# Performance work log

Measured on AMD Instinct MI355X. Metric: run time of the kernel, lower is better.

## Reference

```python
import jax, jax.numpy as jnp
import numpy as np

FRAME, PROJ, MID, HID, T, B = 2048, 512, 128, 1024, 48, 512


def _uniform(key, shape, stdv):
    return jax.random.uniform(key, shape, jnp.float32, -stdv, stdv)


def setup_inputs() -> dict:
    key = jax.random.key(0)
    ks = jax.random.split(key, 16)
    sp = 1.0 / np.sqrt(FRAME)   # frame_embed init
    s1 = 1.0 / np.sqrt(HID)     # LSTMCell init (1/sqrt(hidden))
    sbd = 1.0 / np.sqrt(PROJ)   # BoundaryDetector init (1/sqrt(i_features))
    return {
        "video_feats": jax.random.normal(ks[0], (B, T, FRAME), jnp.float32),
        # frame_embed: Linear(frame_size, projected_size)
        "We": _uniform(ks[1], (PROJ, FRAME), sp),
        "be": _uniform(ks[2], (PROJ,), sp),
        # lstm1: LSTMCell(projected, hidden) with bias
        "W1_ih": _uniform(ks[3], (4 * HID, PROJ), s1),
        "W1_hh": _uniform(ks[4], (4 * HID, HID), s1),
        "b1_ih": _uniform(ks[5], (4 * HID,), s1),
        "b1_hh": _uniform(ks[6], (4 * HID,), s1),
        # lstm2: LSTMCell(hidden, hidden), bias=False
        "W2_ih": _uniform(ks[7], (4 * HID, HID), s1),
        "W2_hh": _uniform(ks[8], (4 * HID, HID), s1),
        # BoundaryDetector params
        "Wsi": _uniform(ks[9], (MID, PROJ), sbd),
        "Wsh": _uniform(ks[10], (MID, HID), sbd),
        "bbd": _uniform(ks[11], (MID,), sbd),
        "vs": _uniform(ks[12], (1, MID), sbd),
    }


def _lstm_cell(x, h, c, W_ih, W_hh, b):
    gates = x @ W_ih.T + h @ W_hh.T + b  # [B, 4H]
    i, f, g, o = jnp.split(gates, 4, axis=-1)  # PyTorch gate order i,f,g,o
    i, f, o = jax.nn.sigmoid(i), jax.nn.sigmoid(f), jax.nn.sigmoid(o)
    g = jnp.tanh(g)
    c_new = f * c + i * g
    h_new = o * jnp.tanh(c_new)
    return h_new, c_new


def _binary_gate(z):
    # eval mode: threshold 0.5; straight-through identity backward
    hard = (z > 0.5).astype(z.dtype)
    return z + jax.lax.stop_gradient(hard - z)


def reference(video_feats, We, be, W1_ih, W1_hh, b1_ih, b1_hh, W2_ih, W2_hh, Wsi, Wsh, bbd, vs):
    bsz = video_feats.shape[0]
    # frame embedding (dropout is identity in eval mode)
    v = video_feats @ We.T + be  # [B, T, PROJ]
    v_t = jnp.swapaxes(v, 0, 1)  # [T, B, PROJ]
    b1 = b1_ih + b1_hh
    zeros = jnp.zeros((bsz, HID), video_feats.dtype)

    def step(carry, vt):
        h1, c1, h2, c2 = carry
        z = jax.nn.sigmoid((vt @ Wsi.T + h1 @ Wsh.T + bbd) @ vs.T)  # [B, 1]
        s = _binary_gate(z)
        h1n, c1n = _lstm_cell(vt, h1, c1, W1_ih, W1_hh, b1)
        h2n, c2n = _lstm_cell(h1n * s, h2, c2, W2_ih, W2_hh, 0.0)
        h1n = h1n * (1.0 - s)
        c1n = c1n * (1.0 - s)
        return (h1n, c1n, h2n, c2n), None

    (h1, _, _, _), _ = jax.lax.scan(step, (zeros, zeros, zeros, zeros), v_t)
    return h1
```

## Files before the change

kernel.cpp:

```cpp
#include <hip/hip_runtime.h>

#define B_     512
#define T_     48
#define FRAME_ 2048
#define PROJ_  512
#define MID_   128
#define HID_   1024
#define G4_    4096

typedef unsigned short u16;
typedef __bf16 bf16x8 __attribute__((ext_vector_type(8)));
typedef float  f32x4  __attribute__((ext_vector_type(4)));

__device__ __forceinline__ float sigmoidf_(float x) {
    return 1.0f / (1.0f + expf(-x));
}
__device__ __forceinline__ u16 f2bf_rn(float f) {
    unsigned int u = __float_as_uint(f);
    u += 0x7fffu + ((u >> 16) & 1u);
    return (u16)(u >> 16);
}
__device__ __forceinline__ float bf2f(u16 s) {
    return __uint_as_float(((unsigned int)s) << 16);
}
__device__ __forceinline__ void gld16(const void* g, void* l) {
    __builtin_amdgcn_global_load_lds((const __attribute__((address_space(1))) void*)g,
                                     (__attribute__((address_space(3))) void*)l, 16, 0, 0);
}
__device__ __forceinline__ uint4 pack8(const u16* h) {
    return make_uint4((unsigned)h[0] | ((unsigned)h[1] << 16),
                      (unsigned)h[2] | ((unsigned)h[3] << 16),
                      (unsigned)h[4] | ((unsigned)h[5] << 16),
                      (unsigned)h[6] | ((unsigned)h[7] << 16));
}

__global__ void wvec_kernel(const float* __restrict__ Wsi, const float* __restrict__ Wsh,
                            const float* __restrict__ vs,
                            double* __restrict__ wsi_vd, float* __restrict__ wsh_v)
{
    const int gid = blockIdx.x * 256 + threadIdx.x;
    if (gid < 512) {
        double s = 0.0;
        for (int mi = 0; mi < MID_; ++mi)
            s += (double)vs[mi] * (double)Wsi[(size_t)mi * PROJ_ + gid];
        wsi_vd[gid] = s;
    } else if (gid < 1536) {
        const int k = gid - 512;
        double s = 0.0;
        for (int mi = 0; mi < MID_; ++mi)
            s += (double)vs[mi] * (double)Wsh[(size_t)mi * HID_ + k];
        wsh_v[k] = (float)s;
    }
}

__global__ void cc_kernel(const float* __restrict__ be, const double* __restrict__ wsi_vd,
                          const float* __restrict__ vs, const float* __restrict__ bbd,
                          double* __restrict__ cc)
{
    __shared__ double red[256];
    const int tid = threadIdx.x;
    double s = 0.0;
    for (int p = tid; p < PROJ_; p += 256) s += (double)be[p] * wsi_vd[p];
    red[tid] = s;
    __syncthreads();
    for (int st = 128; st > 0; st >>= 1) {
        if (tid < st) red[tid] += red[tid + st];
        __syncthreads();
    }
    if (tid == 0) {
        double b = 0.0;
        for (int mi = 0; mi < MID_; ++mi) b += (double)vs[mi] * (double)bbd[mi];
        cc[0] = red[0] + b;
    }
}

__global__ void u_kernel(const float* __restrict__ We, const double* __restrict__ wsi_vd,
                         double* __restrict__ u)
{
    const int f = blockIdx.x * 256 + threadIdx.x;
    double s = 0.0;
    for (int p = 0; p < PROJ_; ++p)
        s += wsi_vd[p] * (double)We[(size_t)p * FRAME_ + f];
    u[f] = s;
}

__global__ __launch_bounds__(256)
void vidpack_kernel(const float* __restrict__ video, const double* __restrict__ u,
                    const double* __restrict__ cc,
                    u16* __restrict__ phi, u16* __restrict__ plo,
                    float* __restrict__ Lv)
{
    __shared__ double red[16][17];
    const int tid = threadIdx.x;
    const int r   = tid & 15, kq = tid >> 4;
    const int row = blockIdx.x * 16 + r;
    const float* vr = video + (size_t)row * FRAME_;
    double s = 0.0;
#pragma unroll
    for (int j = 0; j < 16; ++j) {
        const int k0 = kq * 128 + j * 8;
        const float4 a = *(const float4*)&vr[k0];
        const float4 b = *(const float4*)&vr[k0 + 4];
        const float f[8] = {a.x, a.y, a.z, a.w, b.x, b.y, b.z, b.w};
        s += (double)f[0]*u[k0+0] + (double)f[1]*u[k0+1] + (double)f[2]*u[k0+2]
           + (double)f[3]*u[k0+3] + (double)f[4]*u[k0+4] + (double)f[5]*u[k0+5]
           + (double)f[6]*u[k0+6] + (double)f[7]*u[k0+7];
        u16 h[8], l[8];
#pragma unroll
        for (int e = 0; e < 8; ++e) {
            h[e] = f2bf_rn(f[e]);
            l[e] = f2bf_rn(f[e] - bf2f(h[e]));
        }
        const int g = kq * 16 + j;
        const size_t off = ((size_t)g * 24576 + row) * 16;
        *(uint4*)((char*)phi + off) = pack8(h);
        *(uint4*)((char*)plo + off) = pack8(l);
    }
    red[r][kq] = s;
    __syncthreads();
    if (tid < 16) {
        double t = 0.0;
#pragma unroll
        for (int q = 0; q < 16; ++q) t += red[tid][q];
        const int rw = blockIdx.x * 16 + tid;
        Lv[(rw % T_) * B_ + rw / T_] = (float)(t + cc[0]);
    }
}

__global__ void wepack_kernel(const float* __restrict__ We,
                              u16* __restrict__ phi, u16* __restrict__ plo)
{
    const int kk = blockIdx.x, by = blockIdx.y, tid = threadIdx.x;
#pragma unroll
    for (int pass = 0; pass < 2; ++pass) {
        const int g = tid + pass * 256;
        const int ko = g >> 7, n = g & 127;
        const int p = by * 128 + n;
        const int k = kk * 32 + ko * 8;
        const float4 a = *(const float4*)&We[(size_t)p * FRAME_ + k];
        const float4 b = *(const float4*)&We[(size_t)p * FRAME_ + k + 4];
        const float f[8] = {a.x, a.y, a.z, a.w, b.x, b.y, b.z, b.w};
        u16 h[8], l[8];
#pragma unroll
        for (int e = 0; e < 8; ++e) {
            h[e] = f2bf_rn(f[e]);
            l[e] = f2bf_rn(f[e] - bf2f(h[e]));
        }
        const size_t off = (((size_t)by * 64 + kk) * 512 + g) * 16;
        *(uint4*)((char*)phi + off) = pack8(h);
        *(uint4*)((char*)plo + off) = pack8(l);
    }
}

__global__ void wihpack_kernel(const float* __restrict__ Wih,
                               u16* __restrict__ phi, u16* __restrict__ plo)
{
    const int kk = blockIdx.x, by = blockIdx.y, tid = threadIdx.x;
#pragma unroll
    for (int pass = 0; pass < 2; ++pass) {
        const int g = tid + pass * 256;
        const int ko = g >> 7, n = g & 127;
        const int gate = n & 3, hl = n >> 2;
        const int srow = gate * HID_ + by * 32 + hl;
        const int k = kk * 32 + ko * 8;
        const float4 a = *(const float4*)&Wih[(size_t)srow * PROJ_ + k];
        const float4 b = *(const float4*)&Wih[(size_t)srow * PROJ_ + k + 4];
        const float f[8] = {a.x, a.y, a.z, a.w, b.x, b.y, b.z, b.w};
        u16 h[8], l[8];
#pragma unroll
        for (int e = 0; e < 8; ++e) {
            h[e] = f2bf_rn(f[e]);
            l[e] = f2bf_rn(f[e] - bf2f(h[e]));
        }
        const size_t off = (((size_t)by * 16 + kk) * 512 + g) * 16;
        *(uint4*)((char*)phi + off) = pack8(h);
        *(uint4*)((char*)plo + off) = pack8(l);
    }
}

__global__ void whhpack_kernel(const float* __restrict__ Whh,
                               u16* __restrict__ phi, u16* __restrict__ plo)
{
    const int kk = blockIdx.x, by = blockIdx.y, tid = threadIdx.x;
#pragma unroll
    for (int pass = 0; pass < 2; ++pass) {
        const int g = tid + pass * 256;
        const int ko = g >> 7, n = g & 127;
        const int gate = n & 3, hl = n >> 2;
        const int srow = gate * HID_ + by * 32 + hl;
        const int k = kk * 32 + ko * 8;
        const float4 a = *(const float4*)&Whh[(size_t)srow * HID_ + k];
        const float4 b = *(const float4*)&Whh[(size_t)srow * HID_ + k + 4];
        const float f[8] = {a.x, a.y, a.z, a.w, b.x, b.y, b.z, b.w};
        u16 h[8], l[8];
#pragma unroll
        for (int e = 0; e < 8; ++e) {
            h[e] = f2bf_rn(f[e]);
            l[e] = f2bf_rn(f[e] - bf2f(h[e]));
        }
        const size_t off = (((size_t)by * 32 + kk) * 512 + g) * 16;
        *(uint4*)((char*)phi + off) = pack8(h);
        *(uint4*)((char*)plo + off) = pack8(l);
    }
}

__global__ void b1g_kernel(const float* __restrict__ bih, const float* __restrict__ bhh,
                           float* __restrict__ b1g)
{
    const int n = blockIdx.x * 256 + threadIdx.x;
    const int by = n >> 7, nl = n & 127;
    const int gate = nl & 3, hl = nl >> 2;
    const int src = gate * HID_ + by * 32 + hl;
    b1g[n] = bih[src] + bhh[src];
}


__global__ __launch_bounds__(256, 2)
void embed_mfma_kernel(const u16* __restrict__ Ahi_g, const u16* __restrict__ Alo_g,
                       const u16* __restrict__ Bhi_g, const u16* __restrict__ Blo_g,
                       const float* __restrict__ be,
                       u16* __restrict__ vphi, u16* __restrict__ vplo)
{
    __shared__ char smem[65536];
    const int tid = threadIdx.x;
    const int xcd = blockIdx.x & 7, s_ = blockIdx.x >> 3;
    const int by = s_ & 3, bx = xcd * 24 + (s_ >> 2);
    const int n0 = by * 128, row0 = bx * 128;
    const int w = tid >> 6, l = tid & 63, lm = l & 15, ko4 = l >> 4;
    const int wr = (w >> 1) * 64, wc = (w & 1) * 64;

    const char* aS[4]; const char* bS[4]; int loff[4];
#pragma unroll
    for (int i = 0; i < 4; ++i) {
        const int j = w * 4 + i;
        const int ip = (j & 7) * 64 + l;
        const int ko = ip >> 7, rc = ip & 127;
        const char* ab = (j >> 3) ? (const char*)Alo_g : (const char*)Ahi_g;
        aS[i] = ab + ((size_t)ko * 24576 + row0 + rc) * 16;
        const char* bb = (j >> 3) ? (const char*)Blo_g : (const char*)Bhi_g;
        bS[i] = bb + (size_t)by * 524288 + (size_t)ip * 16;
        loff[i] = j * 1024 + l * 16;
    }

    f32x4 acc[4][4] = {};
#pragma unroll
    for (int i = 0; i < 4; ++i) {
        gld16(aS[i], smem + loff[i]);
        gld16(bS[i], smem + 16384 + loff[i]);
    }

#pragma unroll 2
    for (int kk = 0; kk < 64; ++kk) {
        if (kk + 1 < 64) {
            const int bo = ((kk + 1) & 1) * 32768;
#pragma unroll
            for (int i = 0; i < 4; ++i) {
                gld16(aS[i] + (size_t)(kk + 1) * 1572864, smem + bo + loff[i]);
                gld16(bS[i] + (size_t)(kk + 1) * 8192,    smem + bo + 16384 + loff[i]);
            }
            asm volatile("s_waitcnt vmcnt(8)\ns_barrier" ::: "memory");
        } else {
            asm volatile("s_waitcnt vmcnt(0)\ns_barrier" ::: "memory");
        }
        __builtin_amdgcn_sched_barrier(0);

        const char* rb = smem + (kk & 1) * 32768;
        bf16x8 Ah[4], Al[4], Bh[4], Bl[4];
#pragma unroll
        for (int mt = 0; mt < 4; ++mt) {
            const int idx = (ko4 * 128 + wr + mt * 16 + lm) * 16;
            Ah[mt] = *(const bf16x8*)(rb + idx);
            Al[mt] = *(const bf16x8*)(rb + 8192 + idx);
        }
#pragma unroll
        for (int nt = 0; nt < 4; ++nt) {
            const int idx = (ko4 * 128 + wc + nt * 16 + lm) * 16;
            Bh[nt] = *(const bf16x8*)(rb + 16384 + idx);
            Bl[nt] = *(const bf16x8*)(rb + 24576 + idx);
        }
        asm volatile("s_waitcnt lgkmcnt(0)\ns_barrier" ::: "memory");
        __builtin_amdgcn_sched_barrier(0);
#pragma unroll
        for (int mt = 0; mt < 4; ++mt)
#pragma unroll
            for (int nt = 0; nt < 4; ++nt) {
                acc[mt][nt] = __builtin_amdgcn_mfma_f32_16x16x32_bf16(Ah[mt], Bh[nt], acc[mt][nt], 0, 0, 0);
                acc[mt][nt] = __builtin_amdgcn_mfma_f32_16x16x32_bf16(Ah[mt], Bl[nt], acc[mt][nt], 0, 0, 0);
                acc[mt][nt] = __builtin_amdgcn_mfma_f32_16x16x32_bf16(Al[mt], Bh[nt], acc[mt][nt], 0, 0, 0);
            }
    }

    __syncthreads();
    float* S = (float*)smem;
#pragma unroll
    for (int h = 0; h < 2; ++h) {
        if ((w >> 1) == h) {
#pragma unroll
            for (int mt = 0; mt < 4; ++mt)
#pragma unroll
                for (int nt = 0; nt < 4; ++nt)
#pragma unroll
                    for (int r = 0; r < 4; ++r)
                        S[(mt * 16 + ko4 * 4 + r) * 132 + wc + nt * 16 + lm] = acc[mt][nt][r];
        }
        __syncthreads();
#pragma unroll
        for (int i = 0; i < 4; ++i) {
            const int task = tid * 4 + i;
            const int m = task >> 4, gr = task & 15;
            const int p0 = n0 + gr * 8;
            const float4 s0 = *(const float4*)&S[m * 132 + gr * 8];
            const float4 s1 = *(const float4*)&S[m * 132 + gr * 8 + 4];
            const float4 e0 = *(const float4*)&be[p0];
            const float4 e1 = *(const float4*)&be[p0 + 4];
            const float o[8] = {s0.x + e0.x, s0.y + e0.y, s0.z + e0.z, s0.w + e0.w,
                                s1.x + e1.x, s1.y + e1.y, s1.z + e1.z, s1.w + e1.w};
            u16 hb[8], lb[8];
#pragma unroll
            for (int e = 0; e < 8; ++e) {
                hb[e] = f2bf_rn(o[e]);
                lb[e] = f2bf_rn(o[e] - bf2f(hb[e]));
            }
            const int R = row0 + h * 64 + m;
            const int t = R % T_, b = R / T_;
            const size_t off = (size_t)t * 524288 + (((size_t)(p0 >> 3)) * 512 + b) * 16;
            *(uint4*)((char*)vphi + off) = pack8(hb);
            *(uint4*)((char*)vplo + off) = pack8(lb);
        }
        __syncthreads();
    }
}

__global__ __launch_bounds__(256, 2)
void gx_mfma_kernel(const u16* __restrict__ vphi, const u16* __restrict__ vplo,
                    const u16* __restrict__ Wihhi, const u16* __restrict__ Wihlo,
                    const float* __restrict__ b1g, float* __restrict__ Gx)
{
    __shared__ char smem[65536];
    const int tid = threadIdx.x;
    const int xcd = blockIdx.x & 7, s_ = blockIdx.x >> 3;
    const int by = s_ / 24, bx = xcd * 24 + (s_ % 24);
    const int t2 = bx >> 2, b0 = (bx & 3) * 128;
    const int n0 = by * 128;
    const int w = tid >> 6, l = tid & 63, lm = l & 15, ko4 = l >> 4;
    const int wr = (w >> 1) * 64, wc = (w & 1) * 64;

    const char* aS[4]; const char* bS[4]; int loff[4];
#pragma unroll
    for (int i = 0; i < 4; ++i) {
        const int j = w * 4 + i;
        const int ip = (j & 7) * 64 + l;
        const int ko = ip >> 7, rc = ip & 127;
        const char* ab = ((j >> 3) ? (const char*)vplo : (const char*)vphi)
                         + (size_t)t2 * 524288;
        aS[i] = ab + ((size_t)ko * 512 + b0 + rc) * 16;
        const char* bb = (j >> 3) ? (const char*)Wihlo : (const char*)Wihhi;
        bS[i] = bb + (size_t)by * 131072 + (size_t)ip * 16;
        loff[i] = j * 1024 + l * 16;
    }

    f32x4 acc[4][4] = {};
#pragma unroll
    for (int i = 0; i < 4; ++i) {
        gld16(aS[i], smem + loff[i]);
        gld16(bS[i], smem + 16384 + loff[i]);
    }

#pragma unroll 2
    for (int kk = 0; kk < 16; ++kk) {
        if (kk + 1 < 16) {
            const int bo = ((kk + 1) & 1) * 32768;
#pragma unroll
            for (int i = 0; i < 4; ++i) {
                gld16(aS[i] + (size_t)(kk + 1) * 32768, smem + bo + loff[i]);
                gld16(bS[i] + (size_t)(kk + 1) * 8192,  smem + bo + 16384 + loff[i]);
            }
            asm volatile("s_waitcnt vmcnt(8)\ns_barrier" ::: "memory");
        } else {
            asm volatile("s_waitcnt vmcnt(0)\ns_barrier" ::: "memory");
        }
        __builtin_amdgcn_sched_barrier(0);

        const char* rb = smem + (kk & 1) * 32768;
        bf16x8 Ah[4], Al[4], Bh[4], Bl[4];
#pragma unroll
        for (int mt = 0; mt < 4; ++mt) {
            const int idx = (ko4 * 128 + wr + mt * 16 + lm) * 16;
            Ah[mt] = *(const bf16x8*)(rb + idx);
            Al[mt] = *(const bf16x8*)(rb + 8192 + idx);
        }
#pragma unroll
        for (int nt = 0; nt < 4; ++nt) {
            const int idx = (ko4 * 128 + wc + nt * 16 + lm) * 16;
            Bh[nt] = *(const bf16x8*)(rb + 16384 + idx);
            Bl[nt] = *(const bf16x8*)(rb + 24576 + idx);
        }
        asm volatile("s_waitcnt lgkmcnt(0)\ns_barrier" ::: "memory");
        __builtin_amdgcn_sched_barrier(0);
#pragma unroll
        for (int mt = 0; mt < 4; ++mt)
#pragma unroll
            for (int nt = 0; nt < 4; ++nt) {
                acc[mt][nt] = __builtin_amdgcn_mfma_f32_16x16x32_bf16(Ah[mt], Bh[nt], acc[mt][nt], 0, 0, 0);
                acc[mt][nt] = __builtin_amdgcn_mfma_f32_16x16x32_bf16(Ah[mt], Bl[nt], acc[mt][nt], 0, 0, 0);
                acc[mt][nt] = __builtin_amdgcn_mfma_f32_16x16x32_bf16(Al[mt], Bh[nt], acc[mt][nt], 0, 0, 0);
            }
    }

    float bg[4];
#pragma unroll
    for (int nt = 0; nt < 4; ++nt) bg[nt] = b1g[n0 + wc + nt * 16 + lm];
    float* gbase = Gx + ((size_t)t2 * 512 + b0) * 4096 + n0;
#pragma unroll
    for (int mt = 0; mt < 4; ++mt)
#pragma unroll
        for (int r = 0; r < 4; ++r) {
            const int row = wr + mt * 16 + ko4 * 4 + r;
            float* rp = gbase + (size_t)row * 4096 + wc;
#pragma unroll
            for (int nt = 0; nt < 4; ++nt)
                rp[nt * 16 + lm] = acc[mt][nt][r] + bg[nt];
        }
}

__global__ __launch_bounds__(512, 2)
void lstm_mfma_kernel(const u16* __restrict__ hhi,  const u16* __restrict__ hlo,
                      const u16* __restrict__ Whhhi, const u16* __restrict__ Whhlo,
                      const float* __restrict__ Gxt,
                      const float* __restrict__ Lv_t,
                      const float* __restrict__ Pin,
                      float* __restrict__ Pout,
                      const float* __restrict__ wsh_v,
                      float* __restrict__ c1, float* __restrict__ h1o,
                      u16* __restrict__ hhio, u16* __restrict__ hloo)
{
    __shared__ char smem[34048];
    float* keepsm = (float*)(smem + 33792);
    const int tid = threadIdx.x;
    const int bid = blockIdx.x;
    const int xcd = bid & 7, slot = bid >> 3;
    const int by  = xcd * 4 + (slot & 3);
    const int bx  = slot >> 2;
    const int b0  = bx * 64;
    const int w = tid >> 6, l = tid & 63, lm = l & 15, ko4 = l >> 4;
    const int wr = (w >> 2) * 32, wc = (w & 3) * 32;
    const int t8 = tid & 255;
    const int koA = t8 >> 6, am = t8 & 63;

    if (tid < 64) {
        double s = (double)Lv_t[b0 + tid];
#pragma unroll
        for (int j = 0; j < 32; ++j) s += (double)Pin[j * B_ + b0 + tid];
        keepsm[tid] = (s > 0.0) ? 0.0f : 1.0f;
    }

    const char* aH = (const char*)(tid < 256 ? hhi : hlo)
                     + ((size_t)koA * 512 + b0 + am) * 16;
    const char* bh = (const char*)Whhhi + (size_t)by * 262144
                     + ((size_t)(ko4 * 128 + wc + lm)) * 16;
    const char* bl = (const char*)Whhlo + (size_t)by * 262144
                     + ((size_t)(ko4 * 128 + wc + lm)) * 16;
    char* lbase = smem + (tid >> 8) * 4096 + t8 * 16;

    f32x4 acc[2][2] = {};
    bf16x8 nBh[2], nBl[2], cBh[2], cBl[2], fAh[2], fAl[2];

    gld16(aH, lbase);
    gld16(aH + 32768, lbase + 8192);
#pragma unroll
    for (int nt = 0; nt < 2; ++nt) {
        nBh[nt] = *(const bf16x8*)(bh + nt * 256);
        nBl[nt] = *(const bf16x8*)(bl + nt * 256);
    }

#pragma unroll
    for (int kk = 0; kk < 32; ++kk) {
        if (kk == 31) asm volatile("s_waitcnt vmcnt(4)\ns_barrier" ::: "memory");
        else          asm volatile("s_waitcnt vmcnt(5)\ns_barrier" ::: "memory");
        __builtin_amdgcn_sched_barrier(0);
#pragma unroll
        for (int nt = 0; nt < 2; ++nt) { cBh[nt] = nBh[nt]; cBl[nt] = nBl[nt]; }
        const char* rb = smem + (kk & 3) * 8192;
#pragma unroll
        for (int mt = 0; mt < 2; ++mt) {
            fAh[mt] = *(const bf16x8*)(rb + (ko4 * 64 + wr + mt * 16 + lm) * 16);
            fAl[mt] = *(const bf16x8*)(rb + 4096 + (ko4 * 64 + wr + mt * 16 + lm) * 16);
        }
        if (kk + 1 < 32) {
#pragma unroll
            for (int nt = 0; nt < 2; ++nt) {
                nBh[nt] = *(const bf16x8*)(bh + (size_t)(kk + 1) * 8192 + nt * 256);
                nBl[nt] = *(const bf16x8*)(bl + (size_t)(kk + 1) * 8192 + nt * 256);
            }
        }
        if (kk + 2 < 32) gld16(aH + (size_t)(kk + 2) * 32768, lbase + ((kk + 2) & 3) * 8192);
#pragma unroll
        for (int mt = 0; mt < 2; ++mt)
#pragma unroll
            for (int nt = 0; nt < 2; ++nt) {
                acc[mt][nt] = __builtin_amdgcn_mfma_f32_16x16x32_bf16(fAh[mt], cBh[nt], acc[mt][nt], 0, 0, 0);
                acc[mt][nt] = __builtin_amdgcn_mfma_f32_16x16x32_bf16(fAh[mt], cBl[nt], acc[mt][nt], 0, 0, 0);
                acc[mt][nt] = __builtin_amdgcn_mfma_f32_16x16x32_bf16(fAl[mt], cBh[nt], acc[mt][nt], 0, 0, 0);
            }
    }
    asm volatile("s_waitcnt lgkmcnt(0)" ::: "memory");
    __builtin_amdgcn_sched_barrier(0);

    const int h_l = tid & 31, rg = tid >> 5;
    const int hg  = by * 32 + h_l;
    float4 gx[4];
#pragma unroll
    for (int i = 0; i < 4; ++i)
        gx[i] = *(const float4*)&Gxt[((size_t)b0 + rg * 4 + i) * 4096 + by * 128 + h_l * 4];

    __syncthreads();
    float* S = (float*)smem;
#pragma unroll
    for (int mt = 0; mt < 2; ++mt)
#pragma unroll
        for (int nt = 0; nt < 2; ++nt) {
            const int col = wc + nt * 16 + lm;
#pragma unroll
            for (int r = 0; r < 4; ++r) {
                const int row = wr + mt * 16 + ko4 * 4 + r;
                S[row * 132 + col] = acc[mt][nt][r];
            }
        }
    __syncthreads();

    const float wv = wsh_v[hg];
    const size_t hgbase = (((size_t)by * 4 + (h_l >> 3)) * 512) * 16 + (h_l & 7) * 2;
#pragma unroll
    for (int i = 0; i < 4; ++i) {
        const int m = rg * 4 + i;
        const int b = b0 + m;
        const float4 g4 = *(const float4*)&S[m * 132 + h_l * 4];
        const float i_ = sigmoidf_(g4.x + gx[i].x);
        const float f_ = sigmoidf_(g4.y + gx[i].y);
        const float g_ = tanhf(g4.z + gx[i].z);
        const float o_ = sigmoidf_(g4.w + gx[i].w);
        const size_t off = (size_t)b * HID_ + hg;
        float cn = f_ * c1[off] + i_ * g_;
        float hn = o_ * tanhf(cn);
        const float kp = keepsm[m];
        cn *= kp; hn *= kp;
        c1[off] = cn;
        if (h1o) h1o[off] = hn;
        const u16 hb = f2bf_rn(hn);
        const size_t hoff = hgbase + (size_t)b * 16;
        *(u16*)((char*)hhio + hoff) = hb;
        *(u16*)((char*)hloo + hoff) = f2bf_rn(hn - bf2f(hb));
        float pr = hn * wv;
        pr += __shfl_xor(pr, 16);
        pr += __shfl_xor(pr, 8);
        pr += __shfl_xor(pr, 4);
        pr += __shfl_xor(pr, 2);
        pr += __shfl_xor(pr, 1);
        if (h_l == 0) Pout[by * B_ + b] = pr;
    }
}

extern "C" void kernel_launch(void* const* d_in, const int* in_sizes, int n_in,
                              void* d_out, int out_size, void* d_ws, size_t ws_size,
                              hipStream_t stream)
{
    const float* video = (const float*)d_in[0];
    const float* We    = (const float*)d_in[1];
    const float* be    = (const float*)d_in[2];
    const float* W1_ih = (const float*)d_in[3];
    const float* W1_hh = (const float*)d_in[4];
    const float* b1_ih = (const float*)d_in[5];
    const float* b1_hh = (const float*)d_in[6];
    const float* Wsi   = (const float*)d_in[9];
    const float* Wsh   = (const float*)d_in[10];
    const float* bbd   = (const float*)d_in[11];
    const float* vs    = (const float*)d_in[12];
    float* out = (float*)d_out;

    char* p = (char*)d_ws;
    auto alloc = [&](size_t bytes) { char* r = p; p += (bytes + 255) & ~(size_t)255; return r; };
    u16* vidhi = (u16*)alloc((size_t)24576 * FRAME_ * 2);
    u16* vidlo = (u16*)alloc((size_t)24576 * FRAME_ * 2);
    u16* vphi  = (u16*)alloc((size_t)T_ * B_ * PROJ_ * 2);
    u16* vplo  = (u16*)alloc((size_t)T_ * B_ * PROJ_ * 2);
    u16* Wehi  = (u16*)alloc((size_t)PROJ_ * FRAME_ * 2);
    u16* Welo  = (u16*)alloc((size_t)PROJ_ * FRAME_ * 2);
    u16* Wihhi = (u16*)alloc((size_t)G4_ * PROJ_ * 2);
    u16* Wihlo = (u16*)alloc((size_t)G4_ * PROJ_ * 2);
    u16* Whhhi = (u16*)alloc((size_t)G4_ * HID_ * 2);
    u16* Whhlo = (u16*)alloc((size_t)G4_ * HID_ * 2);
    float* Gx  = (float*)alloc((size_t)T_ * B_ * G4_ * 4);
    float* c1  = (float*)alloc((size_t)B_ * HID_ * 4);
    u16* hhiA  = (u16*)alloc((size_t)B_ * HID_ * 2);
    u16* hhiB  = (u16*)alloc((size_t)B_ * HID_ * 2);
    u16* hloA  = (u16*)alloc((size_t)B_ * HID_ * 2);
    u16* hloB  = (u16*)alloc((size_t)B_ * HID_ * 2);
    double* wsi_vd = (double*)alloc(512 * 8);
    double* ud     = (double*)alloc(2048 * 8);
    double* ccd    = (double*)alloc(256);
    float* wsh_v = (float*)alloc(1024 * 4);
    float* Lv    = (float*)alloc((size_t)T_ * B_ * 4);
    float* PA    = (float*)alloc(32 * B_ * 4);
    float* PB    = (float*)alloc(32 * B_ * 4);
    float* b1g   = (float*)alloc(G4_ * 4);

    hipMemsetAsync(c1,   0, (size_t)B_ * HID_ * 4, stream);
    hipMemsetAsync(hhiA, 0, (size_t)B_ * HID_ * 2, stream);
    hipMemsetAsync(hloA, 0, (size_t)B_ * HID_ * 2, stream);
    hipMemsetAsync(PA,   0, 32 * B_ * 4, stream);

    b1g_kernel<<<16, 256, 0, stream>>>(b1_ih, b1_hh, b1g);
    wvec_kernel<<<6, 256, 0, stream>>>(Wsi, Wsh, vs, wsi_vd, wsh_v);
    cc_kernel<<<1, 256, 0, stream>>>(be, wsi_vd, vs, bbd, ccd);
    u_kernel<<<8, 256, 0, stream>>>(We, wsi_vd, ud);
    wepack_kernel<<<dim3(64, 4), 256, 0, stream>>>(We, Wehi, Welo);
    wihpack_kernel<<<dim3(16, 32), 256, 0, stream>>>(W1_ih, Wihhi, Wihlo);
    whhpack_kernel<<<dim3(32, 32), 256, 0, stream>>>(W1_hh, Whhhi, Whhlo);
    vidpack_kernel<<<1536, 256, 0, stream>>>(video, ud, ccd, vidhi, vidlo, Lv);
    embed_mfma_kernel<<<768, 256, 0, stream>>>(vidhi, vidlo, Wehi, Welo, be, vphi, vplo);
    gx_mfma_kernel<<<6144, 256, 0, stream>>>(vphi, vplo, Wihhi, Wihlo, b1g, Gx);

    u16* hhi_in = hhiA; u16* hhi_out = hhiB;
    u16* hlo_in = hloA; u16* hlo_out = hloB;
    float* Pin = PA; float* Pout = PB;

    for (int t = 0; t < T_; ++t) {
        float* ho = (t == T_ - 1) ? out : nullptr;
        lstm_mfma_kernel<<<256, 512, 0, stream>>>(hhi_in, hlo_in, Whhhi, Whhlo,
                                                  Gx + (size_t)t * B_ * G4_,
                                                  Lv + t * B_, Pin, Pout, wsh_v,
                                                  c1, ho, hhi_out, hlo_out);
        { u16* tmp = hhi_in; hhi_in = hhi_out; hhi_out = tmp; }
        { u16* tmp = hlo_in; hlo_in = hlo_out; hlo_out = tmp; }
        { float* tmp = Pin; Pin = Pout; Pout = tmp; }
    }
}
```

Before: 1.611 ms.

## Double K-step per barrier in LSTM recurrent GEMM and remap gx block order

Result: slower. 1.653 ms (+2.6%).

```diff
diff --git a/kernel.cpp b/kernel.cpp
--- a/kernel.cpp
+++ b/kernel.cpp
@@ -339,8 +339,9 @@
     __shared__ char smem[65536];
     const int tid = threadIdx.x;
     const int xcd = blockIdx.x & 7, s_ = blockIdx.x >> 3;
-    const int by = s_ / 24, bx = xcd * 24 + (s_ % 24);
-    const int t2 = bx >> 2, b0 = (bx & 3) * 128;
+    const int by = s_ & 31;
+    const int tile = xcd * 24 + (s_ >> 5);
+    const int t2 = tile >> 2, b0 = (tile & 3) * 128;
     const int n0 = by * 128;
     const int w = tid >> 6, l = tid & 63, lm = l & 15, ko4 = l >> 4;
     const int wr = (w >> 1) * 64, wc = (w & 1) * 64;
@@ -434,8 +435,8 @@
                       float* __restrict__ c1, float* __restrict__ h1o,
                       u16* __restrict__ hhio, u16* __restrict__ hloo)
 {
-    __shared__ char smem[34048];
-    float* keepsm = (float*)(smem + 33792);
+    __shared__ char smem[65792];
+    float* keepsm = (float*)(smem + 65536);
     const int tid = threadIdx.x;
     const int bid = blockIdx.x;
     const int xcd = bid & 7, slot = bid >> 3;
@@ -463,45 +464,64 @@
     char* lbase = smem + (tid >> 8) * 4096 + t8 * 16;
 
     f32x4 acc[2][2] = {};
-    bf16x8 nBh[2], nBl[2], cBh[2], cBl[2], fAh[2], fAl[2];
-
-    gld16(aH, lbase);
-    gld16(aH + 32768, lbase + 8192);
-#pragma unroll
-    for (int nt = 0; nt < 2; ++nt) {
-        nBh[nt] = *(const bf16x8*)(bh + nt * 256);
-        nBl[nt] = *(const bf16x8*)(bl + nt * 256);
-    }
-
-#pragma unroll
-    for (int kk = 0; kk < 32; ++kk) {
-        if (kk == 31) asm volatile("s_waitcnt vmcnt(4)\ns_barrier" ::: "memory");
-        else          asm volatile("s_waitcnt vmcnt(5)\ns_barrier" ::: "memory");
+    bf16x8 nBh[2][2], nBl[2][2], cBh[2][2], cBl[2][2], fAh[2][2], fAl[2][2];
+
+    gld16(aH + (size_t)0 * 32768, lbase);
+    gld16(aH + (size_t)1 * 32768, lbase + 8192);
+    gld16(aH + (size_t)2 * 32768, lbase + 16384);
+    gld16(aH + (size_t)3 * 32768, lbase + 16384 + 8192);
+#pragma unroll
+    for (int h = 0; h < 2; ++h)
+#pragma unroll
+        for (int nt = 0; nt < 2; ++nt) {
+            nBh[h][nt] = *(const bf16x8*)(bh + (size_t)h * 8192 + nt * 256);
+            nBl[h][nt] = *(const bf16x8*)(bl + (size_t)h * 8192 + nt * 256);
+        }
+
+#pragma unroll
+    for (int kk = 0; kk < 16; ++kk) {
+        if (kk == 15) asm volatile("s_waitcnt vmcnt(8)\ns_barrier" ::: "memory");
+        else          asm volatile("s_waitcnt vmcnt(10)\ns_barrier" ::: "memory");
         __builtin_amdgcn_sched_barrier(0);
 #pragma unroll
-        for (int nt = 0; nt < 2; ++nt) { cBh[nt] = nBh[nt]; cBl[nt] = nBl[nt]; }
-        const char* rb = smem + (kk & 3) * 8192;
-#pragma unroll
-        for (int mt = 0; mt < 2; ++mt) {
-            fAh[mt] = *(const bf16x8*)(rb + (ko4 * 64 + wr + mt * 16 + lm) * 16);
-            fAl[mt] = *(const bf16x8*)(rb + 4096 + (ko4 * 64 + wr + mt * 16 + lm) * 16);
-        }
-        if (kk + 1 < 32) {
+        for (int h = 0; h < 2; ++h)
 #pragma unroll
             for (int nt = 0; nt < 2; ++nt) {
-                nBh[nt] = *(const bf16x8*)(bh + (size_t)(kk + 1) * 8192 + nt * 256);
-                nBl[nt] = *(const bf16x8*)(bl + (size_t)(kk + 1) * 8192 + nt * 256);
-            }
-        }
-        if (kk + 2 < 32) gld16(aH + (size_t)(kk + 2) * 32768, lbase + ((kk + 2) & 3) * 8192);
-#pragma unroll
-        for (int mt = 0; mt < 2; ++mt)
-#pragma unroll
-            for (int nt = 0; nt < 2; ++nt) {
-                acc[mt][nt] = __builtin_amdgcn_mfma_f32_16x16x32_bf16(fAh[mt], cBh[nt], acc[mt][nt], 0, 0, 0);
-                acc[mt][nt] = __builtin_amdgcn_mfma_f32_16x16x32_bf16(fAh[mt], cBl[nt], acc[mt][nt], 0, 0, 0);
-                acc[mt][nt] = __builtin_amdgcn_mfma_f32_16x16x32_bf16(fAl[mt], cBh[nt], acc[mt][nt], 0, 0, 0);
-            }
+                cBh[h][nt] = nBh[h][nt]; cBl[h][nt] = nBl[h][nt];
+            }
+        const char* rb = smem + (kk & 3) * 16384;
+#pragma unroll
+        for (int h = 0; h < 2; ++h)
+#pragma unroll
+            for (int mt = 0; mt < 2; ++mt) {
+                const int idx = (ko4 * 64 + wr + mt * 16 + lm) * 16;
+                fAh[h][mt] = *(const bf16x8*)(rb + h * 8192 + idx);
+                fAl[h][mt] = *(const bf16x8*)(rb + h * 8192 + 4096 + idx);
+            }
+        if (kk + 1 < 16) {
+#pragma unroll
+            for (int h = 0; h < 2; ++h)
+#pragma unroll
+                for (int nt = 0; nt < 2; ++nt) {
+                    nBh[h][nt] = *(const bf16x8*)(bh + (size_t)(2 * (kk + 1) + h) * 8192 + nt * 256);
+                    nBl[h][nt] = *(const bf16x8*)(bl + (size_t)(2 * (kk + 1) + h) * 8192 + nt * 256);
+                }
+        }
+        if (kk + 2 < 16) {
+            char* db = smem + ((kk + 2) & 3) * 16384 + (tid >> 8) * 4096 + t8 * 16;
+            gld16(aH + (size_t)(2 * (kk + 2) + 0) * 32768, db);
+            gld16(aH + (size_t)(2 * (kk + 2) + 1) * 32768, db + 8192);
+        }
+#pragma unroll
+        for (int h = 0; h < 2; ++h)
+#pragma unroll
+            for (int mt = 0; mt < 2; ++mt)
+#pragma unroll
+                for (int nt = 0; nt < 2; ++nt) {
+                    acc[mt][nt] = __builtin_amdgcn_mfma_f32_16x16x32_bf16(fAh[h][mt], cBh[h][nt], acc[mt][nt], 0, 0, 0);
+                    acc[mt][nt] = __builtin_amdgcn_mfma_f32_16x16x32_bf16(fAh[h][mt], cBl[h][nt], acc[mt][nt], 0, 0, 0);
+                    acc[mt][nt] = __builtin_amdgcn_mfma_f32_16x16x32_bf16(fAl[h][mt], cBh[h][nt], acc[mt][nt], 0, 0, 0);
+                }
     }
     asm volatile("s_waitcnt lgkmcnt(0)" ::: "memory");
     __builtin_amdgcn_sched_barrier(0);
```
